# Optimization experiments

Hardware: AMD Instinct MI355X
Metric: run time of the kernel (lower is better)

The kernel has to match this reference:

```python
import jax, jax.numpy as jnp
import numpy as np

N = 50000          # nodes
E = 800000         # edges (avg degree 16)
F = 128            # in_dim = num_hidden*heads = pred_dim
H = 4              # attention heads per layer
D = 32             # num_hidden (per-head dim)
R = 11             # rel_num
L = 2              # num_layers
SCALE = float(1.0 / np.sqrt(D))


def setup_inputs() -> dict:
    key = jax.random.key(0)
    ks = jax.random.split(key, 16)
    inputs = jax.random.normal(ks[0], (N, F), jnp.float32)
    edge_types = jax.random.randint(ks[1], (E,), 0, R)
    src = jax.random.randint(ks[2], (E,), 0, N)
    dst = jax.random.randint(ks[3], (E,), 0, N)
    centrality = jax.random.uniform(ks[4], (N,), jnp.float32)
    rel_emb = jax.random.normal(ks[5], (R, F), jnp.float32) * 0.1
    # stacked per-layer projection weights (both layers have F -> H*D = F)
    Wq = jax.random.normal(ks[6], (L, F, H * D), jnp.float32) * 0.05
    Wk = jax.random.normal(ks[7], (L, F, H * D), jnp.float32) * 0.05
    Wv = jax.random.normal(ks[8], (L, F, H * D), jnp.float32) * 0.05
    We = jax.random.normal(ks[9], (L, F, H * D), jnp.float32) * 0.05
    bq = jnp.zeros((L, H * D), jnp.float32)
    bk = jnp.zeros((L, H * D), jnp.float32)
    bv = jnp.zeros((L, H * D), jnp.float32)
    be = jnp.zeros((L, H * D), jnp.float32)
    W_out = jax.random.normal(ks[10], (H * D, 1), jnp.float32) * 0.05
    b_out = jnp.zeros((1,), jnp.float32)
    gamma = jnp.ones((1,), jnp.float32)
    beta = jnp.zeros((1,), jnp.float32)
    return {"inputs": inputs, "edge_types": edge_types, "src": src, "dst": dst,
            "centrality": centrality, "rel_emb": rel_emb,
            "Wq": Wq, "bq": bq, "Wk": Wk, "bk": bk, "Wv": Wv, "bv": bv,
            "We": We, "be": be, "W_out": W_out, "b_out": b_out,
            "gamma": gamma, "beta": beta}


def _segment_softmax(score, dst, n):
    # score: [E, H]; softmax over incoming edges of each dst node
    m = jax.ops.segment_max(score, dst, num_segments=n)          # [N, H]
    ex = jnp.exp(score - m[dst])                                  # [E, H]
    s = jax.ops.segment_sum(ex, dst, num_segments=n)              # [N, H]
    return ex / (s[dst] + 1e-9)


def reference(inputs, edge_types, src, dst, centrality, rel_emb,
              Wq, bq, Wk, bk, Wv, bv, We, be, W_out, b_out, gamma, beta):
    h = inputs                                   # [N, F]
    ef = rel_emb[edge_types]                     # [E, pred_dim] relational edge embedding
    for l in range(L):
        q = (h @ Wq[l] + bq[l]).reshape(N, H, D)
        k = (h @ Wk[l] + bk[l]).reshape(N, H, D)
        v = (h @ Wv[l] + bv[l]).reshape(N, H, D)
        e = (ef @ We[l] + be[l]).reshape(E, H, D)
        # edge_mode="add": edge features added to keys/values on each edge
        ke = k[src] + e                           # [E, H, D]
        score = jnp.sum(q[dst] * ke, axis=-1) * SCALE   # [E, H]
        attn = _segment_softmax(score, dst, N)          # [E, H]
        msg = attn[:, :, None] * (v[src] + e)           # [E, H, D]
        agg = jax.ops.segment_sum(msg, dst, num_segments=N)  # [N, H, D]
        # identity residual (in_dim == H*D) + ELU activation
        h = jax.nn.elu(agg.reshape(N, H * D) + h)
    logits = h @ W_out + b_out                    # [N, 1]
    logits = jax.nn.relu((centrality * gamma + beta)[:, None] * logits)
    return logits
```

## Files before the change

### kernel.cpp

```cpp
#include <hip/hip_runtime.h>
#include <hip/hip_bf16.h>
#include <math.h>

#define SCALE_C 0.17677669529663687f
#define CAPP 64

typedef short bf16x8 __attribute__((ext_vector_type(8)));
typedef float f32x4 __attribute__((ext_vector_type(4)));
typedef _Float16 h16x2 __attribute__((ext_vector_type(2)));
typedef unsigned u32x4 __attribute__((ext_vector_type(4)));

__device__ __forceinline__ h16x2 bch2(unsigned u) { return __builtin_bit_cast(h16x2, u); }

__device__ __forceinline__ uint4 nt_load16(const void* p) {
  u32x4 v = __builtin_nontemporal_load((const u32x4*)p);
  return __builtin_bit_cast(uint4, v);
}


__global__ __launch_bounds__(256) void prep0_k(
    const float* __restrict__ Wq, const float* __restrict__ Wk, const float* __restrict__ Wv,
    __hip_bfloat16* __restrict__ wf,
    const float* __restrict__ rel_emb, const float* __restrict__ We, const float* __restrict__ be,
    _Float16* __restrict__ re, int R, int reb,
    int* __restrict__ cnt, int N) {
  int b = blockIdx.x;
  if (b < 48) {
    int tid = b * 256 + threadIdx.x;
    int lane = tid & 63;
    int frag = tid >> 6;
    int ks = frag & 3;
    int ct = (frag >> 2) & 7;
    int mat = frag >> 5;
    int l = mat / 3, m = mat % 3;
    const float* W = ((m == 0) ? Wq : (m == 1) ? Wk : Wv) + (size_t)l * 128 * 128;
    int nn = ct * 16 + (lane & 15);
    int k0 = ks * 32 + (lane >> 4) * 8;
    __hip_bfloat16 tmp[8];
    #pragma unroll
    for (int j = 0; j < 8; ++j) tmp[j] = __float2bfloat16(W[(size_t)(k0 + j) * 128 + nn]);
    *(uint4*)&wf[(size_t)frag * 64 * 8 + (size_t)lane * 8] = *(const uint4*)tmp;
  } else if (b < 48 + reb) {
    int idx = (b - 48) * 256 + threadIdx.x;
    int tot = 2 * R * 128;
    if (idx >= tot) return;
    int c = idx & 127;
    int r = (idx >> 7) % R;
    int l = idx / (R * 128);
    const float* W = We + (size_t)l * 128 * 128;
    float acc = be[l * 128 + c];
    #pragma unroll 4
    for (int kk = 0; kk < 128; ++kk) acc += rel_emb[r * 128 + kk] * W[kk * 128 + c];
    re[idx] = (_Float16)acc;
  } else {
    int idx = (b - 48 - reb) * 256 + threadIdx.x;
    if (idx < N) cnt[idx] = 0;
  }
}


__device__ __forceinline__ void qkv_body(
    const float* __restrict__ Xf, const __hip_bfloat16* __restrict__ Xb,
    const __hip_bfloat16* __restrict__ wf,
    const float* __restrict__ bq, const float* __restrict__ bk, const float* __restrict__ bv,
    _Float16* __restrict__ qo, _Float16* __restrict__ kvo, int n, int bid) {
  __shared__ __attribute__((aligned(16))) __hip_bfloat16 xs[32][136];
  __shared__ __attribute__((aligned(16))) _Float16 ot[3][32][136];
  int tid = threadIdx.x;
  int wid = tid >> 6;
  int lane = tid & 63;
  int row0 = bid * 32;
  if (row0 >= n) return;

  for (int idx = tid; idx < 512; idx += 192) {
    int row = idx >> 4, g = idx & 15;
    union { uint4 u; __hip_bfloat16 h[8]; } P;
    P.u = make_uint4(0, 0, 0, 0);
    if (row0 + row < n) {
      if (Xb) {
        P.u = *(const uint4*)(Xb + (size_t)(row0 + row) * 128 + g * 8);
      } else {
        const float* xr = Xf + (size_t)(row0 + row) * 128 + g * 8;
        float4 x0 = *(const float4*)xr;
        float4 x1 = *(const float4*)(xr + 4);
        P.h[0] = __float2bfloat16(x0.x); P.h[1] = __float2bfloat16(x0.y);
        P.h[2] = __float2bfloat16(x0.z); P.h[3] = __float2bfloat16(x0.w);
        P.h[4] = __float2bfloat16(x1.x); P.h[5] = __float2bfloat16(x1.y);
        P.h[6] = __float2bfloat16(x1.z); P.h[7] = __float2bfloat16(x1.w);
      }
    }
    *(uint4*)&xs[row][g * 8] = P.u;
  }
  __syncthreads();

  int cl = lane & 15;
  int quad = lane >> 4;

  bf16x8 afrag[2][4];
  #pragma unroll
  for (int s = 0; s < 2; ++s)
    #pragma unroll
    for (int ks = 0; ks < 4; ++ks)
      afrag[s][ks] = *(const bf16x8*)&xs[s * 16 + cl][quad * 8 + ks * 32];

  const uint4* wfu = (const uint4*)wf;
  const float* bias = (wid == 0) ? bq : (wid == 1) ? bk : bv;
  float scl = (wid == 0) ? SCALE_C : 1.0f;

  #pragma unroll
  for (int ct = 0; ct < 8; ++ct) {
    f32x4 a0 = {0.f, 0.f, 0.f, 0.f}, a1 = {0.f, 0.f, 0.f, 0.f};
    #pragma unroll
    for (int ks = 0; ks < 4; ++ks) {
      uint4 braw = wfu[((size_t)(wid * 8 + ct) * 4 + ks) * 64 + lane];
      bf16x8 bfr = __builtin_bit_cast(bf16x8, braw);
      a0 = __builtin_amdgcn_mfma_f32_16x16x32_bf16(afrag[0][ks], bfr, a0, 0, 0, 0);
      a1 = __builtin_amdgcn_mfma_f32_16x16x32_bf16(afrag[1][ks], bfr, a1, 0, 0, 0);
    }
    int c = ct * 16 + cl;
    float bb = bias[c];
    #pragma unroll
    for (int r = 0; r < 4; ++r) {
      ot[wid][quad * 4 + r][c]      = (_Float16)((a0[r] + bb) * scl);
      ot[wid][16 + quad * 4 + r][c] = (_Float16)((a1[r] + bb) * scl);
    }
  }

  if (wid == 0) {
    #pragma unroll
    for (int it = 0; it < 8; ++it) {
      int idx = it * 64 + lane;
      int row = idx >> 4, g = idx & 15;
      if (row0 + row < n)
        *(uint4*)&qo[(size_t)(row0 + row) * 128 + g * 8] = *(const uint4*)&ot[0][row][g * 8];
    }
  } else {
    int off = (wid == 1) ? 0 : 128;
    #pragma unroll
    for (int it = 0; it < 8; ++it) {
      int idx = it * 64 + lane;
      int row = idx >> 4, g = idx & 15;
      if (row0 + row < n)
        *(uint4*)&kvo[(size_t)(row0 + row) * 256 + off + g * 8] = *(const uint4*)&ot[wid][row][g * 8];
    }
  }
}


__global__ __launch_bounds__(192) void qkv1s_k(
    const float* __restrict__ Xf, const __hip_bfloat16* __restrict__ wf,
    const float* __restrict__ bq, const float* __restrict__ bk, const float* __restrict__ bv,
    _Float16* __restrict__ qo, _Float16* __restrict__ kvo, int n, int QB,
    const int* __restrict__ dst, const int* __restrict__ src, const int* __restrict__ etype,
    int E, int* __restrict__ cnt, int* __restrict__ bins) {
  if ((int)blockIdx.x < QB) {
    qkv_body(Xf, nullptr, wf, bq, bk, bv, qo, kvo, n, blockIdx.x);
  } else {
    int e = (blockIdx.x - QB) * 192 + threadIdx.x;
    if (e < E) {
      int d = dst[e];
      int pos = atomicAdd(&cnt[d], 1);
      if (pos < CAPP) bins[(d << 6) + pos] = src[e] | (etype[e] << 20);
    }
  }
}

__global__ __launch_bounds__(192) void qkv2_k(
    const __hip_bfloat16* __restrict__ Xb, const __hip_bfloat16* __restrict__ wf,
    const float* __restrict__ bq, const float* __restrict__ bk, const float* __restrict__ bv,
    _Float16* __restrict__ qo, _Float16* __restrict__ kvo, int n) {
  qkv_body(nullptr, Xb, wf, bq, bk, bv, qo, kvo, n, blockIdx.x);
}


__global__ __launch_bounds__(256) void edge_k(
    const _Float16* __restrict__ qb, const _Float16* __restrict__ kv,
    const _Float16* __restrict__ re,
    const int* __restrict__ bins, const int* __restrict__ cnt,
    const float* __restrict__ h_in_f, const __hip_bfloat16* __restrict__ h_in_b,
    __hip_bfloat16* __restrict__ h_out_b,
    const float* __restrict__ Wout, const float* __restrict__ bout,
    const float* __restrict__ cent, const float* __restrict__ gamma,
    const float* __restrict__ beta, float* __restrict__ outp, int n) {
  int node = blockIdx.x * 4 + (threadIdx.x >> 6);
  if (node >= n) return;
  int lane = threadIdx.x & 63;
  int j = lane & 15;
  int quarter = lane >> 4;
  int rs = node << 6;
  int deg = cnt[node];
  deg = deg < CAPP ? deg : CAPP;
  uint nm1 = (uint)(n - 1);

  uint4 qraw = nt_load16((const uint4*)(qb + ((size_t)node << 7)) + j);

  float4 h0, h1;
  if (h_in_b) {
    uint4 hraw = nt_load16((const uint4*)(h_in_b + ((size_t)node << 7)) + j);
    h0.x = __uint_as_float(hraw.x << 16); h0.y = __uint_as_float(hraw.x & 0xffff0000u);
    h0.z = __uint_as_float(hraw.y << 16); h0.w = __uint_as_float(hraw.y & 0xffff0000u);
    h1.x = __uint_as_float(hraw.z << 16); h1.y = __uint_as_float(hraw.z & 0xffff0000u);
    h1.z = __uint_as_float(hraw.w << 16); h1.w = __uint_as_float(hraw.w & 0xffff0000u);
  } else {
    const float4* hrow = (const float4*)h_in_f + ((uint)node * 32u + (uint)(j * 2));
    uint4 t0 = nt_load16(hrow);
    uint4 t1 = nt_load16(hrow + 1);
    h0.x = __uint_as_float(t0.x); h0.y = __uint_as_float(t0.y);
    h0.z = __uint_as_float(t0.z); h0.w = __uint_as_float(t0.w);
    h1.x = __uint_as_float(t1.x); h1.y = __uint_as_float(t1.y);
    h1.z = __uint_as_float(t1.z); h1.w = __uint_as_float(t1.w);
  }

  h16x2 q01 = bch2(qraw.x), q23 = bch2(qraw.y), q45 = bch2(qraw.z), q67 = bch2(qraw.w);
  float qa0 = (float)q01.x, qa1 = (float)q01.y;
  float qa2 = (float)q23.x, qa3 = (float)q23.y;
  float qa4 = (float)q45.x, qa5 = (float)q45.y;
  float qa6 = (float)q67.x, qa7 = (float)q67.y;

  float ssum = 0.f;
  float acc0 = 0.f, acc1 = 0.f, acc2 = 0.f, acc3 = 0.f;
  float acc4 = 0.f, acc5 = 0.f, acc6 = 0.f, acc7 = 0.f;

  int nit = (deg + 3) >> 2;
  nit = (nit + 1) & ~1;

  const uint4* kvb  = (const uint4*)kv + (uint)j;
  const uint4* rebp = (const uint4*)re + (uint)j;

  auto loadstage = [&](int pk, uint4& rk, uint4& rv, uint4& rr) {
    uint s = (uint)pk & 0xFFFFFu; s = s < nm1 ? s : nm1;
    uint t = (uint)pk >> 20;
    const uint4* kp = kvb + s * 32u;
    rk = kp[0];
    rv = kp[16];
    rr = rebp[t * 16u];
  };
  auto accum = [&](uint4 rk, uint4 rv, uint4 rr, int eidx) {
    h16x2 r01 = bch2(rr.x), r23 = bch2(rr.y), r45 = bch2(rr.z), r67 = bch2(rr.w);
    h16x2 kr01 = bch2(rk.x) + r01;
    h16x2 kr23 = bch2(rk.y) + r23;
    h16x2 kr45 = bch2(rk.z) + r45;
    h16x2 kr67 = bch2(rk.w) + r67;
    h16x2 vr01 = bch2(rv.x) + r01;
    h16x2 vr23 = bch2(rv.y) + r23;
    h16x2 vr45 = bch2(rv.z) + r45;
    h16x2 vr67 = bch2(rv.w) + r67;
    float pA = qa0 * (float)kr01.x;
    pA += qa1 * (float)kr01.y;
    pA += qa2 * (float)kr23.x;
    pA += qa3 * (float)kr23.y;
    float pB = qa4 * (float)kr45.x;
    pB += qa5 * (float)kr45.y;
    pB += qa6 * (float)kr67.x;
    pB += qa7 * (float)kr67.y;
    float p = pA + pB;
    p += __shfl_xor(p, 1);
    p += __shfl_xor(p, 2);
    float w = (eidx < deg) ? __expf(p) : 0.f;
    ssum += w;
    acc0 += w * (float)vr01.x;
    acc1 += w * (float)vr01.y;
    acc2 += w * (float)vr23.x;
    acc3 += w * (float)vr23.y;
    acc4 += w * (float)vr45.x;
    acc5 += w * (float)vr45.y;
    acc6 += w * (float)vr67.x;
    acc7 += w * (float)vr67.y;
  };

  uint4 a0, a1, ar, b0, b1, br;
  loadstage(bins[rs + quarter], a0, a1, ar);
  loadstage(bins[rs + quarter + 4], b0, b1, br);

  for (int i = 0; i < nit; i += 2) {
    bool more = (i + 2) < nit;
    int e2a = 4 * i + 8 + quarter;  e2a = e2a < 63 ? e2a : 63;
    int e2b = 4 * i + 12 + quarter; e2b = e2b < 63 ? e2b : 63;
    int pkA2 = bins[rs + e2a];
    int pkB2 = bins[rs + e2b];
    accum(a0, a1, ar, 4 * i + quarter);
    if (more) loadstage(pkA2, a0, a1, ar);
    accum(b0, b1, br, 4 * i + 4 + quarter);
    if (more) loadstage(pkB2, b0, b1, br);
  }

  ssum += __shfl_xor(ssum, 16); ssum += __shfl_xor(ssum, 32);
  acc0 += __shfl_xor(acc0, 16); acc0 += __shfl_xor(acc0, 32);
  acc1 += __shfl_xor(acc1, 16); acc1 += __shfl_xor(acc1, 32);
  acc2 += __shfl_xor(acc2, 16); acc2 += __shfl_xor(acc2, 32);
  acc3 += __shfl_xor(acc3, 16); acc3 += __shfl_xor(acc3, 32);
  acc4 += __shfl_xor(acc4, 16); acc4 += __shfl_xor(acc4, 32);
  acc5 += __shfl_xor(acc5, 16); acc5 += __shfl_xor(acc5, 32);
  acc6 += __shfl_xor(acc6, 16); acc6 += __shfl_xor(acc6, 32);
  acc7 += __shfl_xor(acc7, 16); acc7 += __shfl_xor(acc7, 32);
  if (quarter != 0) return;

  float inv = __builtin_amdgcn_rcpf(ssum + 1e-9f);
  float x0 = acc0 * inv + h0.x;
  float x1 = acc1 * inv + h0.y;
  float x2 = acc2 * inv + h0.z;
  float x3 = acc3 * inv + h0.w;
  float x4 = acc4 * inv + h1.x;
  float x5 = acc5 * inv + h1.y;
  float x6 = acc6 * inv + h1.z;
  float x7 = acc7 * inv + h1.w;
  x0 = x0 > 0.f ? x0 : __expf(x0) - 1.f;
  x1 = x1 > 0.f ? x1 : __expf(x1) - 1.f;
  x2 = x2 > 0.f ? x2 : __expf(x2) - 1.f;
  x3 = x3 > 0.f ? x3 : __expf(x3) - 1.f;
  x4 = x4 > 0.f ? x4 : __expf(x4) - 1.f;
  x5 = x5 > 0.f ? x5 : __expf(x5) - 1.f;
  x6 = x6 > 0.f ? x6 : __expf(x6) - 1.f;
  x7 = x7 > 0.f ? x7 : __expf(x7) - 1.f;
  if (outp == nullptr) {
    union { uint4 u; __hip_bfloat16 hh[8]; } P;
    P.hh[0] = __float2bfloat16(x0); P.hh[1] = __float2bfloat16(x1);
    P.hh[2] = __float2bfloat16(x2); P.hh[3] = __float2bfloat16(x3);
    P.hh[4] = __float2bfloat16(x4); P.hh[5] = __float2bfloat16(x5);
    P.hh[6] = __float2bfloat16(x6); P.hh[7] = __float2bfloat16(x7);
    *((uint4*)(h_out_b + ((size_t)node << 7)) + j) = P.u;
  } else {
    const float4* wrow = (const float4*)Wout + (uint)(j * 2);
    float4 w0 = wrow[0], w1 = wrow[1];
    float pp = x0 * w0.x + x1 * w0.y + x2 * w0.z + x3 * w0.w
             + x4 * w1.x + x5 * w1.y + x6 * w1.z + x7 * w1.w;
    pp += __shfl_xor(pp, 1);
    pp += __shfl_xor(pp, 2);
    pp += __shfl_xor(pp, 4);
    pp += __shfl_xor(pp, 8);
    if (lane == 0) {
      float lg = pp + bout[0];
      lg *= (cent[node] * gamma[0] + beta[0]);
      outp[node] = fmaxf(lg, 0.f);
    }
  }
}


extern "C" void kernel_launch(void* const* d_in, const int* in_sizes, int n_in,
                              void* d_out, int out_size, void* d_ws, size_t ws_size,
                              hipStream_t stream) {
  const float* inputs  = (const float*)d_in[0];
  const int*   etype   = (const int*)d_in[1];
  const int*   src     = (const int*)d_in[2];
  const int*   dst     = (const int*)d_in[3];
  const float* cent    = (const float*)d_in[4];
  const float* rel_emb = (const float*)d_in[5];
  const float* Wq      = (const float*)d_in[6];
  const float* bq      = (const float*)d_in[7];
  const float* Wk      = (const float*)d_in[8];
  const float* bk      = (const float*)d_in[9];
  const float* Wv      = (const float*)d_in[10];
  const float* bv      = (const float*)d_in[11];
  const float* We      = (const float*)d_in[12];
  const float* be      = (const float*)d_in[13];
  const float* Wout    = (const float*)d_in[14];
  const float* bout    = (const float*)d_in[15];
  const float* gamma   = (const float*)d_in[16];
  const float* beta    = (const float*)d_in[17];
  float* out = (float*)d_out;

  const int N = in_sizes[0] / 128;
  const int E = in_sizes[1];
  const int R = in_sizes[5] / 128;

  _Float16* re = (_Float16*)d_ws;
  __hip_bfloat16* hb = (__hip_bfloat16*)(re + 2 * (size_t)R * 128);
  _Float16* qb = (_Float16*)(hb + (size_t)N * 128);
  _Float16* kv = qb + (size_t)N * 128;
  __hip_bfloat16* wf = (__hip_bfloat16*)(kv + (size_t)N * 256);
  int* cnt  = (int*)(wf + 6 * 16384);
  int* bins = cnt + N;

  int reb = (2 * R * 128 + 255) / 256;
  int CB  = (N + 255) / 256;
  prep0_k<<<48 + reb + CB, 256, 0, stream>>>(Wq, Wk, Wv, wf, rel_emb, We, be, re, R, reb,
                                             cnt, N);

  int QB = (N + 31) / 32;
  int SB = (E + 191) / 192;
  int eb = (N + 3) / 4;
  qkv1s_k<<<QB + SB, 192, 0, stream>>>(inputs, wf, bq, bk, bv, qb, kv, N, QB,
                                       dst, src, etype, E, cnt, bins);
  edge_k<<<eb, 256, 0, stream>>>(qb, kv, re, bins, cnt,
                                 inputs, nullptr, hb,
                                 Wout, bout, cent, gamma, beta, nullptr, N);
  qkv2_k<<<QB, 192, 0, stream>>>(hb, wf + (size_t)3 * 16384,
                                 bq + 128, bk + 128, bv + 128, qb, kv, N);
  edge_k<<<eb, 256, 0, stream>>>(qb, kv, re + (size_t)R * 128, bins, cnt,
                                 nullptr, hb, nullptr,
                                 Wout, bout, cent, gamma, beta, out, N);
}
```

Baseline: 320.0 us.

## Fuse all stages into one persistent cooperative kernel with grid syncs

Replaces the five separate launches (prep, qkv+scatter, edge, qkv2, edge) with a single persistent cooperative kernel sized to full occupancy. Stages are separated by grid-wide barriers instead of kernel boundaries, and blocks loop over work items. The QKV tile is reworked for 256 threads so each wave computes six column tiles spanning the three matrices. This removes launch gaps and tail effects but adds grid-sync cost, caps occupancy at four blocks per CU, and forces both edge stages into the shared-memory footprint that the QKV tile needs.

```diff
diff --git a/kernel.cpp b/kernel.cpp
--- a/kernel.cpp
+++ b/kernel.cpp
@@ -1,6 +1,9 @@
 #include <hip/hip_runtime.h>
+#include <hip/hip_cooperative_groups.h>
 #include <hip/hip_bf16.h>
 #include <math.h>
+
+namespace cg = cooperative_groups;
 
 #define SCALE_C 0.17677669529663687f
 #define CAPP 64
@@ -17,79 +20,49 @@
   return __builtin_bit_cast(uint4, v);
 }
 
-
-__global__ __launch_bounds__(256) void prep0_k(
-    const float* __restrict__ Wq, const float* __restrict__ Wk, const float* __restrict__ Wv,
-    __hip_bfloat16* __restrict__ wf,
-    const float* __restrict__ rel_emb, const float* __restrict__ We, const float* __restrict__ be,
-    _Float16* __restrict__ re, int R, int reb,
-    int* __restrict__ cnt, int N) {
-  int b = blockIdx.x;
-  if (b < 48) {
-    int tid = b * 256 + threadIdx.x;
-    int lane = tid & 63;
-    int frag = tid >> 6;
-    int ks = frag & 3;
-    int ct = (frag >> 2) & 7;
-    int mat = frag >> 5;
-    int l = mat / 3, m = mat % 3;
-    const float* W = ((m == 0) ? Wq : (m == 1) ? Wk : Wv) + (size_t)l * 128 * 128;
-    int nn = ct * 16 + (lane & 15);
-    int k0 = ks * 32 + (lane >> 4) * 8;
-    __hip_bfloat16 tmp[8];
-    #pragma unroll
-    for (int j = 0; j < 8; ++j) tmp[j] = __float2bfloat16(W[(size_t)(k0 + j) * 128 + nn]);
-    *(uint4*)&wf[(size_t)frag * 64 * 8 + (size_t)lane * 8] = *(const uint4*)tmp;
-  } else if (b < 48 + reb) {
-    int idx = (b - 48) * 256 + threadIdx.x;
-    int tot = 2 * R * 128;
-    if (idx >= tot) return;
-    int c = idx & 127;
-    int r = (idx >> 7) % R;
-    int l = idx / (R * 128);
-    const float* W = We + (size_t)l * 128 * 128;
-    float acc = be[l * 128 + c];
-    #pragma unroll 4
-    for (int kk = 0; kk < 128; ++kk) acc += rel_emb[r * 128 + kk] * W[kk * 128 + c];
-    re[idx] = (_Float16)acc;
-  } else {
-    int idx = (b - 48 - reb) * 256 + threadIdx.x;
-    if (idx < N) cnt[idx] = 0;
-  }
-}
-
-
-__device__ __forceinline__ void qkv_body(
+struct Params {
+  const float *Wq, *Wk, *Wv, *We, *be, *rel_emb, *inputs;
+  const float *bq, *bk, *bv, *Wout, *bout, *cent, *gamma, *beta;
+  const int *etype, *src, *dst;
+  float* out;
+  _Float16 *re, *qb, *kv;
+  __hip_bfloat16 *hb, *wf;
+  int *cnt, *bins;
+  int N, E, R, reb, CB, SB, QB, EB;
+};
+
+
+__device__ __forceinline__ void qkv_tile(
     const float* __restrict__ Xf, const __hip_bfloat16* __restrict__ Xb,
     const __hip_bfloat16* __restrict__ wf,
     const float* __restrict__ bq, const float* __restrict__ bk, const float* __restrict__ bv,
-    _Float16* __restrict__ qo, _Float16* __restrict__ kvo, int n, int bid) {
-  __shared__ __attribute__((aligned(16))) __hip_bfloat16 xs[32][136];
-  __shared__ __attribute__((aligned(16))) _Float16 ot[3][32][136];
+    _Float16* __restrict__ qo, _Float16* __restrict__ kvo, int n, int bid,
+    __hip_bfloat16 (*xs)[136], _Float16 (*ot)[32][136]) {
   int tid = threadIdx.x;
   int wid = tid >> 6;
   int lane = tid & 63;
   int row0 = bid * 32;
-  if (row0 >= n) return;
-
-  for (int idx = tid; idx < 512; idx += 192) {
+
+  #pragma unroll
+  for (int k = 0; k < 2; ++k) {
+    int idx = tid + k * 256;
     int row = idx >> 4, g = idx & 15;
-    union { uint4 u; __hip_bfloat16 h[8]; } P;
-    P.u = make_uint4(0, 0, 0, 0);
+    union { uint4 u; __hip_bfloat16 h[8]; } Pk;
+    Pk.u = make_uint4(0, 0, 0, 0);
     if (row0 + row < n) {
       if (Xb) {
-        P.u = *(const uint4*)(Xb + (size_t)(row0 + row) * 128 + g * 8);
+        Pk.u = *(const uint4*)(Xb + (size_t)(row0 + row) * 128 + g * 8);
       } else {
         const float* xr = Xf + (size_t)(row0 + row) * 128 + g * 8;
         float4 x0 = *(const float4*)xr;
         float4 x1 = *(const float4*)(xr + 4);
-        P.h[0] = __float2bfloat16(x0.x); P.h[1] = __float2bfloat16(x0.y);
-        P.h[2] = __float2bfloat16(x0.z); P.h[3] = __float2bfloat16(x0.w);
-        P.h[4] = __float2bfloat16(x1.x); P.h[5] = __float2bfloat16(x1.y);
-        P.h[6] = __float2bfloat16(x1.z); P.h[7] = __float2bfloat16(x1.w);
+        Pk.h[0] = __float2bfloat16(x0.x); Pk.h[1] = __float2bfloat16(x0.y);
+        Pk.h[2] = __float2bfloat16(x0.z); Pk.h[3] = __float2bfloat16(x0.w);
+        Pk.h[4] = __float2bfloat16(x1.x); Pk.h[5] = __float2bfloat16(x1.y);
+        Pk.h[6] = __float2bfloat16(x1.z); Pk.h[7] = __float2bfloat16(x1.w);
       }
     }
-    *(uint4*)&xs[row][g * 8] = P.u;
+    *(uint4*)&xs[row][g * 8] = Pk.u;
   }
   __syncthreads();
 
@@ -104,76 +77,49 @@
       afrag[s][ks] = *(const bf16x8*)&xs[s * 16 + cl][quad * 8 + ks * 32];
 
   const uint4* wfu = (const uint4*)wf;
-  const float* bias = (wid == 0) ? bq : (wid == 1) ? bk : bv;
-  float scl = (wid == 0) ? SCALE_C : 1.0f;
 
   #pragma unroll
-  for (int ct = 0; ct < 8; ++ct) {
+  for (int uu = 0; uu < 6; ++uu) {
+    int u = wid * 6 + uu;
+    int mat = u >> 3, ct = u & 7;
     f32x4 a0 = {0.f, 0.f, 0.f, 0.f}, a1 = {0.f, 0.f, 0.f, 0.f};
     #pragma unroll
     for (int ks = 0; ks < 4; ++ks) {
-      uint4 braw = wfu[((size_t)(wid * 8 + ct) * 4 + ks) * 64 + lane];
+      uint4 braw = wfu[((size_t)(mat * 8 + ct) * 4 + ks) * 64 + lane];
       bf16x8 bfr = __builtin_bit_cast(bf16x8, braw);
       a0 = __builtin_amdgcn_mfma_f32_16x16x32_bf16(afrag[0][ks], bfr, a0, 0, 0, 0);
       a1 = __builtin_amdgcn_mfma_f32_16x16x32_bf16(afrag[1][ks], bfr, a1, 0, 0, 0);
     }
     int c = ct * 16 + cl;
+    const float* bias = (mat == 0) ? bq : (mat == 1) ? bk : bv;
     float bb = bias[c];
+    float scl = (mat == 0) ? SCALE_C : 1.0f;
     #pragma unroll
     for (int r = 0; r < 4; ++r) {
-      ot[wid][quad * 4 + r][c]      = (_Float16)((a0[r] + bb) * scl);
-      ot[wid][16 + quad * 4 + r][c] = (_Float16)((a1[r] + bb) * scl);
-    }
-  }
-
-  if (wid == 0) {
-    #pragma unroll
-    for (int it = 0; it < 8; ++it) {
-      int idx = it * 64 + lane;
-      int row = idx >> 4, g = idx & 15;
-      if (row0 + row < n)
-        *(uint4*)&qo[(size_t)(row0 + row) * 128 + g * 8] = *(const uint4*)&ot[0][row][g * 8];
-    }
-  } else {
-    int off = (wid == 1) ? 0 : 128;
-    #pragma unroll
-    for (int it = 0; it < 8; ++it) {
-      int idx = it * 64 + lane;
-      int row = idx >> 4, g = idx & 15;
-      if (row0 + row < n)
-        *(uint4*)&kvo[(size_t)(row0 + row) * 256 + off + g * 8] = *(const uint4*)&ot[wid][row][g * 8];
+      ot[mat][quad * 4 + r][c]      = (_Float16)((a0[r] + bb) * scl);
+      ot[mat][16 + quad * 4 + r][c] = (_Float16)((a1[r] + bb) * scl);
+    }
+  }
+  __syncthreads();
+
+  #pragma unroll
+  for (int k = 0; k < 6; ++k) {
+    int idx = tid + k * 256;
+    int mat = idx >> 9;
+    int rem = idx & 511;
+    int row = rem >> 4, g = rem & 15;
+    if (row0 + row < n) {
+      uint4 val = *(const uint4*)&ot[mat][row][g * 8];
+      if (mat == 0)
+        *(uint4*)&qo[(size_t)(row0 + row) * 128 + g * 8] = val;
+      else
+        *(uint4*)&kvo[(size_t)(row0 + row) * 256 + ((mat == 1) ? 0 : 128) + g * 8] = val;
     }
   }
 }
 
 
-__global__ __launch_bounds__(192) void qkv1s_k(
-    const float* __restrict__ Xf, const __hip_bfloat16* __restrict__ wf,
-    const float* __restrict__ bq, const float* __restrict__ bk, const float* __restrict__ bv,
-    _Float16* __restrict__ qo, _Float16* __restrict__ kvo, int n, int QB,
-    const int* __restrict__ dst, const int* __restrict__ src, const int* __restrict__ etype,
-    int E, int* __restrict__ cnt, int* __restrict__ bins) {
-  if ((int)blockIdx.x < QB) {
-    qkv_body(Xf, nullptr, wf, bq, bk, bv, qo, kvo, n, blockIdx.x);
-  } else {
-    int e = (blockIdx.x - QB) * 192 + threadIdx.x;
-    if (e < E) {
-      int d = dst[e];
-      int pos = atomicAdd(&cnt[d], 1);
-      if (pos < CAPP) bins[(d << 6) + pos] = src[e] | (etype[e] << 20);
-    }
-  }
-}
-
-__global__ __launch_bounds__(192) void qkv2_k(
-    const __hip_bfloat16* __restrict__ Xb, const __hip_bfloat16* __restrict__ wf,
-    const float* __restrict__ bq, const float* __restrict__ bk, const float* __restrict__ bv,
-    _Float16* __restrict__ qo, _Float16* __restrict__ kvo, int n) {
-  qkv_body(nullptr, Xb, wf, bq, bk, bv, qo, kvo, n, blockIdx.x);
-}
-
-
-__global__ __launch_bounds__(256) void edge_k(
+__device__ __forceinline__ void edge_node(
     const _Float16* __restrict__ qb, const _Float16* __restrict__ kv,
     const _Float16* __restrict__ re,
     const int* __restrict__ bins, const int* __restrict__ cnt,
@@ -181,9 +127,7 @@
     __hip_bfloat16* __restrict__ h_out_b,
     const float* __restrict__ Wout, const float* __restrict__ bout,
     const float* __restrict__ cent, const float* __restrict__ gamma,
-    const float* __restrict__ beta, float* __restrict__ outp, int n) {
-  int node = blockIdx.x * 4 + (threadIdx.x >> 6);
-  if (node >= n) return;
+    const float* __restrict__ beta, float* __restrict__ outp, int n, int node) {
   int lane = threadIdx.x & 63;
   int j = lane & 15;
   int quarter = lane >> 4;
@@ -293,46 +237,126 @@
   acc5 += __shfl_xor(acc5, 16); acc5 += __shfl_xor(acc5, 32);
   acc6 += __shfl_xor(acc6, 16); acc6 += __shfl_xor(acc6, 32);
   acc7 += __shfl_xor(acc7, 16); acc7 += __shfl_xor(acc7, 32);
-  if (quarter != 0) return;
-
-  float inv = __builtin_amdgcn_rcpf(ssum + 1e-9f);
-  float x0 = acc0 * inv + h0.x;
-  float x1 = acc1 * inv + h0.y;
-  float x2 = acc2 * inv + h0.z;
-  float x3 = acc3 * inv + h0.w;
-  float x4 = acc4 * inv + h1.x;
-  float x5 = acc5 * inv + h1.y;
-  float x6 = acc6 * inv + h1.z;
-  float x7 = acc7 * inv + h1.w;
-  x0 = x0 > 0.f ? x0 : __expf(x0) - 1.f;
-  x1 = x1 > 0.f ? x1 : __expf(x1) - 1.f;
-  x2 = x2 > 0.f ? x2 : __expf(x2) - 1.f;
-  x3 = x3 > 0.f ? x3 : __expf(x3) - 1.f;
-  x4 = x4 > 0.f ? x4 : __expf(x4) - 1.f;
-  x5 = x5 > 0.f ? x5 : __expf(x5) - 1.f;
-  x6 = x6 > 0.f ? x6 : __expf(x6) - 1.f;
-  x7 = x7 > 0.f ? x7 : __expf(x7) - 1.f;
-  if (outp == nullptr) {
-    union { uint4 u; __hip_bfloat16 hh[8]; } P;
-    P.hh[0] = __float2bfloat16(x0); P.hh[1] = __float2bfloat16(x1);
-    P.hh[2] = __float2bfloat16(x2); P.hh[3] = __float2bfloat16(x3);
-    P.hh[4] = __float2bfloat16(x4); P.hh[5] = __float2bfloat16(x5);
-    P.hh[6] = __float2bfloat16(x6); P.hh[7] = __float2bfloat16(x7);
-    *((uint4*)(h_out_b + ((size_t)node << 7)) + j) = P.u;
-  } else {
-    const float4* wrow = (const float4*)Wout + (uint)(j * 2);
-    float4 w0 = wrow[0], w1 = wrow[1];
-    float pp = x0 * w0.x + x1 * w0.y + x2 * w0.z + x3 * w0.w
-             + x4 * w1.x + x5 * w1.y + x6 * w1.z + x7 * w1.w;
-    pp += __shfl_xor(pp, 1);
-    pp += __shfl_xor(pp, 2);
-    pp += __shfl_xor(pp, 4);
-    pp += __shfl_xor(pp, 8);
-    if (lane == 0) {
-      float lg = pp + bout[0];
-      lg *= (cent[node] * gamma[0] + beta[0]);
-      outp[node] = fmaxf(lg, 0.f);
-    }
+
+  if (quarter == 0) {
+    float inv = __builtin_amdgcn_rcpf(ssum + 1e-9f);
+    float x0 = acc0 * inv + h0.x;
+    float x1 = acc1 * inv + h0.y;
+    float x2 = acc2 * inv + h0.z;
+    float x3 = acc3 * inv + h0.w;
+    float x4 = acc4 * inv + h1.x;
+    float x5 = acc5 * inv + h1.y;
+    float x6 = acc6 * inv + h1.z;
+    float x7 = acc7 * inv + h1.w;
+    x0 = x0 > 0.f ? x0 : __expf(x0) - 1.f;
+    x1 = x1 > 0.f ? x1 : __expf(x1) - 1.f;
+    x2 = x2 > 0.f ? x2 : __expf(x2) - 1.f;
+    x3 = x3 > 0.f ? x3 : __expf(x3) - 1.f;
+    x4 = x4 > 0.f ? x4 : __expf(x4) - 1.f;
+    x5 = x5 > 0.f ? x5 : __expf(x5) - 1.f;
+    x6 = x6 > 0.f ? x6 : __expf(x6) - 1.f;
+    x7 = x7 > 0.f ? x7 : __expf(x7) - 1.f;
+    if (outp == nullptr) {
+      union { uint4 u; __hip_bfloat16 hh[8]; } Pw;
+      Pw.hh[0] = __float2bfloat16(x0); Pw.hh[1] = __float2bfloat16(x1);
+      Pw.hh[2] = __float2bfloat16(x2); Pw.hh[3] = __float2bfloat16(x3);
+      Pw.hh[4] = __float2bfloat16(x4); Pw.hh[5] = __float2bfloat16(x5);
+      Pw.hh[6] = __float2bfloat16(x6); Pw.hh[7] = __float2bfloat16(x7);
+      *((uint4*)(h_out_b + ((size_t)node << 7)) + j) = Pw.u;
+    } else {
+      const float4* wrow = (const float4*)Wout + (uint)(j * 2);
+      float4 w0 = wrow[0], w1 = wrow[1];
+      float pp = x0 * w0.x + x1 * w0.y + x2 * w0.z + x3 * w0.w
+               + x4 * w1.x + x5 * w1.y + x6 * w1.z + x7 * w1.w;
+      pp += __shfl_xor(pp, 1);
+      pp += __shfl_xor(pp, 2);
+      pp += __shfl_xor(pp, 4);
+      pp += __shfl_xor(pp, 8);
+      if (lane == 0) {
+        float lg = pp + bout[0];
+        lg *= (cent[node] * gamma[0] + beta[0]);
+        outp[node] = fmaxf(lg, 0.f);
+      }
+    }
+  }
+}
+
+
+__global__ __launch_bounds__(256, 4) void fused_k(Params p) {
+  __shared__ __attribute__((aligned(16))) __hip_bfloat16 xs[32][136];
+  __shared__ __attribute__((aligned(16))) _Float16 ot[3][32][136];
+  cg::grid_group grid = cg::this_grid();
+  int tid = threadIdx.x;
+
+  for (int b = blockIdx.x; b < 48 + p.reb + p.CB; b += gridDim.x) {
+    if (b < 48) {
+      int t = b * 256 + tid;
+      int lane = t & 63;
+      int frag = t >> 6;
+      int ks = frag & 3;
+      int ct = (frag >> 2) & 7;
+      int mat = frag >> 5;
+      int l = mat / 3, m = mat % 3;
+      const float* W = ((m == 0) ? p.Wq : (m == 1) ? p.Wk : p.Wv) + (size_t)l * 128 * 128;
+      int nn = ct * 16 + (lane & 15);
+      int k0 = ks * 32 + (lane >> 4) * 8;
+      union { uint4 u; __hip_bfloat16 h[8]; } T;
+      #pragma unroll
+      for (int jj = 0; jj < 8; ++jj) T.h[jj] = __float2bfloat16(W[(size_t)(k0 + jj) * 128 + nn]);
+      *(uint4*)&p.wf[(size_t)frag * 64 * 8 + (size_t)lane * 8] = T.u;
+    } else if (b < 48 + p.reb) {
+      int idx = (b - 48) * 256 + tid;
+      int tot = 2 * p.R * 128;
+      if (idx < tot) {
+        int c = idx & 127;
+        int r = (idx >> 7) % p.R;
+        int l = idx / (p.R * 128);
+        const float* W = p.We + (size_t)l * 128 * 128;
+        float acc = p.be[l * 128 + c];
+        #pragma unroll 4
+        for (int kk = 0; kk < 128; ++kk) acc += p.rel_emb[r * 128 + kk] * W[kk * 128 + c];
+        p.re[idx] = (_Float16)acc;
+      }
+    } else {
+      int idx = (b - 48 - p.reb) * 256 + tid;
+      if (idx < p.N) p.cnt[idx] = 0;
+    }
+  }
+  grid.sync();
+
+  for (int v = blockIdx.x; v < p.SB + p.QB; v += gridDim.x) {
+    if (v < p.SB) {
+      int e = v * 256 + tid;
+      if (e < p.E) {
+        int d = p.dst[e];
+        int pos = atomicAdd(&p.cnt[d], 1);
+        if (pos < CAPP) p.bins[(d << 6) + pos] = p.src[e] | (p.etype[e] << 20);
+      }
+    } else {
+      qkv_tile(p.inputs, nullptr, p.wf, p.bq, p.bk, p.bv, p.qb, p.kv, p.N, v - p.SB, xs, ot);
+    }
+  }
+  grid.sync();
+
+  for (int g = blockIdx.x; g < p.EB; g += gridDim.x) {
+    int node = g * 4 + (tid >> 6);
+    if (node < p.N)
+      edge_node(p.qb, p.kv, p.re, p.bins, p.cnt, p.inputs, nullptr, p.hb,
+                p.Wout, p.bout, p.cent, p.gamma, p.beta, nullptr, p.N, node);
+  }
+  grid.sync();
+
+  for (int b = blockIdx.x; b < p.QB; b += gridDim.x) {
+    qkv_tile(nullptr, p.hb, p.wf + (size_t)3 * 16384,
+             p.bq + 128, p.bk + 128, p.bv + 128, p.qb, p.kv, p.N, b, xs, ot);
+  }
+  grid.sync();
+
+  for (int g = blockIdx.x; g < p.EB; g += gridDim.x) {
+    int node = g * 4 + (tid >> 6);
+    if (node < p.N)
+      edge_node(p.qb, p.kv, p.re + (size_t)p.R * 128, p.bins, p.cnt, nullptr, p.hb, nullptr,
+                p.Wout, p.bout, p.cent, p.gamma, p.beta, p.out, p.N, node);
   }
 }
 
@@ -340,54 +364,62 @@
 extern "C" void kernel_launch(void* const* d_in, const int* in_sizes, int n_in,
                               void* d_out, int out_size, void* d_ws, size_t ws_size,
                               hipStream_t stream) {
-  const float* inputs  = (const float*)d_in[0];
-  const int*   etype   = (const int*)d_in[1];
-  const int*   src     = (const int*)d_in[2];
-  const int*   dst     = (const int*)d_in[3];
-  const float* cent    = (const float*)d_in[4];
-  const float* rel_emb = (const float*)d_in[5];
-  const float* Wq      = (const float*)d_in[6];
-  const float* bq      = (const float*)d_in[7];
-  const float* Wk      = (const float*)d_in[8];
-  const float* bk      = (const float*)d_in[9];
-  const float* Wv      = (const float*)d_in[10];
-  const float* bv      = (const float*)d_in[11];
-  const float* We      = (const float*)d_in[12];
-  const float* be      = (const float*)d_in[13];
-  const float* Wout    = (const float*)d_in[14];
-  const float* bout    = (const float*)d_in[15];
-  const float* gamma   = (const float*)d_in[16];
-  const float* beta    = (const float*)d_in[17];
-  float* out = (float*)d_out;
-
-  const int N = in_sizes[0] / 128;
-  const int E = in_sizes[1];
-  const int R = in_sizes[5] / 128;
-
-  _Float16* re = (_Float16*)d_ws;
-  __hip_bfloat16* hb = (__hip_bfloat16*)(re + 2 * (size_t)R * 128);
-  _Float16* qb = (_Float16*)(hb + (size_t)N * 128);
-  _Float16* kv = qb + (size_t)N * 128;
-  __hip_bfloat16* wf = (__hip_bfloat16*)(kv + (size_t)N * 256);
-  int* cnt  = (int*)(wf + 6 * 16384);
-  int* bins = cnt + N;
-
-  int reb = (2 * R * 128 + 255) / 256;
-  int CB  = (N + 255) / 256;
-  prep0_k<<<48 + reb + CB, 256, 0, stream>>>(Wq, Wk, Wv, wf, rel_emb, We, be, re, R, reb,
-                                             cnt, N);
-
-  int QB = (N + 31) / 32;
-  int SB = (E + 191) / 192;
-  int eb = (N + 3) / 4;
-  qkv1s_k<<<QB + SB, 192, 0, stream>>>(inputs, wf, bq, bk, bv, qb, kv, N, QB,
-                                       dst, src, etype, E, cnt, bins);
-  edge_k<<<eb, 256, 0, stream>>>(qb, kv, re, bins, cnt,
-                                 inputs, nullptr, hb,
-                                 Wout, bout, cent, gamma, beta, nullptr, N);
-  qkv2_k<<<QB, 192, 0, stream>>>(hb, wf + (size_t)3 * 16384,
-                                 bq + 128, bk + 128, bv + 128, qb, kv, N);
-  edge_k<<<eb, 256, 0, stream>>>(qb, kv, re + (size_t)R * 128, bins, cnt,
-                                 nullptr, hb, nullptr,
-                                 Wout, bout, cent, gamma, beta, out, N);
+  Params p;
+  p.inputs  = (const float*)d_in[0];
+  p.etype   = (const int*)d_in[1];
+  p.src     = (const int*)d_in[2];
+  p.dst     = (const int*)d_in[3];
+  p.cent    = (const float*)d_in[4];
+  p.rel_emb = (const float*)d_in[5];
+  p.Wq      = (const float*)d_in[6];
+  p.bq      = (const float*)d_in[7];
+  p.Wk      = (const float*)d_in[8];
+  p.bk      = (const float*)d_in[9];
+  p.Wv      = (const float*)d_in[10];
+  p.bv      = (const float*)d_in[11];
+  p.We      = (const float*)d_in[12];
+  p.be      = (const float*)d_in[13];
+  p.Wout    = (const float*)d_in[14];
+  p.bout    = (const float*)d_in[15];
+  p.gamma   = (const float*)d_in[16];
+  p.beta    = (const float*)d_in[17];
+  p.out     = (float*)d_out;
+
+  p.N = in_sizes[0] / 128;
+  p.E = in_sizes[1];
+  p.R = in_sizes[5] / 128;
+
+  p.re = (_Float16*)d_ws;
+  p.hb = (__hip_bfloat16*)(p.re + 2 * (size_t)p.R * 128);
+  p.qb = (_Float16*)(p.hb + (size_t)p.N * 128);
+  p.kv = p.qb + (size_t)p.N * 128;
+  p.wf = (__hip_bfloat16*)(p.kv + (size_t)p.N * 256);
+  p.cnt  = (int*)(p.wf + 6 * 16384);
+  p.bins = p.cnt + p.N;
+
+  p.reb = (2 * p.R * 128 + 255) / 256;
+  p.CB  = (p.N + 255) / 256;
+  p.SB  = (p.E + 255) / 256;
+  p.QB  = (p.N + 31) / 32;
+  p.EB  = (p.N + 3) / 4;
+
+  static int s_nb = 0;
+  if (s_nb == 0) {
+    int occ = 0;
+    hipError_t err = hipOccupancyMaxActiveBlocksPerMultiprocessor(
+        &occ, reinterpret_cast<const void*>(fused_k), 256, 0);
+    if (err != hipSuccess || occ < 1) occ = 1;
+    int cus = 0;
+    hipDeviceProp_t prop;
+    int dev = 0;
+    if (hipGetDevice(&dev) == hipSuccess &&
+        hipGetDeviceProperties(&prop, dev) == hipSuccess)
+      cus = prop.multiProcessorCount;
+    if (cus <= 0) cus = 256;
+    s_nb = occ * cus;
+  }
+
+  void* args[] = { &p };
+  hipLaunchCooperativeKernel(reinterpret_cast<const void*>(fused_k),
+                             dim3(s_nb), dim3(256), args, 0, stream);
 }
```

New measurement: 679.3 us. +112.3%, slower.
